# Optimization experiments

Measured on AMD Instinct MI355X. Metric: run time of the kernel, lower is better.

The kernel has to match this reference:

```python
import jax, jax.numpy as jnp
import numpy as np

C = 256
DF = 8
CQK = C // DF  # 32


def setup_inputs() -> dict:
    key = jax.random.key(0)
    ks = jax.random.split(key, 7)
    s = 0.02
    x = jax.random.normal(ks[0], (4, C, 64, 64), dtype=jnp.float32)
    Wq = jax.random.normal(ks[1], (CQK, C), dtype=jnp.float32) * s
    bq = jnp.zeros((CQK,), dtype=jnp.float32)
    Wk = jax.random.normal(ks[2], (CQK, C), dtype=jnp.float32) * s
    bk = jnp.zeros((CQK,), dtype=jnp.float32)
    Wv = jax.random.normal(ks[3], (C, C), dtype=jnp.float32) * s
    bv = jnp.zeros((C,), dtype=jnp.float32)
    gamma = jnp.ones((1,), dtype=jnp.float32)  # nonzero so output is nontrivial
    return {"x": x, "Wq": Wq, "bq": bq, "Wk": Wk, "bk": bk, "Wv": Wv, "bv": bv, "gamma": gamma}


def reference(x, Wq, bq, Wk, bk, Wv, bv, gamma):
    B, Cc, H, W = x.shape
    # flatten spatial: [B, N, C] with N = H*W
    xf = x.reshape(B, Cc, H * W).transpose(0, 2, 1)
    # 1x1 convs == per-pixel linear projections
    q = jnp.einsum('bnc,dc->bnd', xf, Wq) + bq        # [B, N, Cqk]
    k = jnp.einsum('bnc,dc->bnd', xf, Wk) + bk        # [B, N, Cqk]
    v = jnp.einsum('bnc,dc->bnd', xf, Wv) + bv        # [B, N, C]
    energy = jnp.einsum('bnd,bmd->bnm', q, k)          # [B, N, N], no scale (as in source)
    attn = jax.nn.softmax(energy, axis=-1)
    out = jnp.einsum('bnm,bmc->bnc', attn, v)          # [B, N, C]
    out = out.transpose(0, 2, 1).reshape(B, Cc, H, W)
    return gamma[0] * out
```

## Files before the change

### kernel.cpp

```cpp
#include <hip/hip_runtime.h>
#include <hip/hip_bf16.h>


typedef __attribute__((ext_vector_type(8))) short s8v;
typedef __attribute__((ext_vector_type(4))) float f4v;

#define NPIX 4096
#define CIN 256
#define DQK 32

#if __has_builtin(__builtin_amdgcn_exp2f)
#define EXP2(x) __builtin_amdgcn_exp2f(x)
#else
#define EXP2(x) exp2f(x)
#endif

#if __has_builtin(__builtin_amdgcn_s_waitcnt)
#define LGKM0_BARRIER() { __builtin_amdgcn_s_waitcnt(0xC07F); __builtin_amdgcn_s_barrier(); }
#else
#define LGKM0_BARRIER() { __asm__ __volatile__("s_waitcnt lgkmcnt(0)\n\ts_barrier" ::: "memory"); }
#endif

static __device__ __forceinline__ unsigned short f2bf(float f) {
    union { float f; unsigned int u; } v; v.f = f;
    unsigned int r = v.u + 0x7FFF + ((v.u >> 16) & 1);
    return (unsigned short)(r >> 16);
}
static __device__ __forceinline__ unsigned int fbits(float f) {
    union { float f; unsigned int u; } v; v.f = f; return v.u;
}

__global__ void wcast_kernel(const float* __restrict__ Wq, const float* __restrict__ bq,
                             const float* __restrict__ Wk, const float* __restrict__ bk,
                             const float* __restrict__ Wv, const float* __restrict__ bv,
                             unsigned short* __restrict__ Wall, float* __restrict__ ball) {
    int row = blockIdx.x;
    int t = threadIdx.x;
    const float* src; const float* bsrc;
    if (row < 32)       { src = Wq + row * 256;        bsrc = bq + row; }
    else if (row < 64)  { src = Wk + (row - 32) * 256; bsrc = bk + (row - 32); }
    else                { src = Wv + (row - 64) * 256; bsrc = bv + (row - 64); }
    Wall[row * 256 + t] = f2bf(src[t]);
    if (t == 0) ball[row] = bsrc[0];
}

__global__ void tcast_kernel(const float* __restrict__ x, unsigned short* __restrict__ xT) {
    __shared__ unsigned short tile[64][65];
    int bidx = blockIdx.x;
    int b    = bidx >> 8;
    int cblk = (bidx >> 6) & 3;
    int nblk = bidx & 63;
    int t = threadIdx.x;
    int c0 = cblk * 64, n0 = nblk * 64;
    const float* xb = x + (size_t)b * CIN * NPIX;
    #pragma unroll
    for (int p = 0; p < 4; p++) {
        int cl = p * 16 + (t >> 4);
        int nl = (t & 15) * 4;
        float4 v = *(const float4*)(xb + (size_t)(c0 + cl) * NPIX + n0 + nl);
        tile[cl][nl + 0] = f2bf(v.x);
        tile[cl][nl + 1] = f2bf(v.y);
        tile[cl][nl + 2] = f2bf(v.z);
        tile[cl][nl + 3] = f2bf(v.w);
    }
    __syncthreads();
    unsigned short* xTb = xT + (size_t)b * NPIX * CIN;
    #pragma unroll
    for (int p = 0; p < 4; p++) {
        int nl = p * 16 + (t >> 4);
        int cl = (t & 15) * 4;
        ushort4 wv;
        wv.x = tile[cl + 0][nl];
        wv.y = tile[cl + 1][nl];
        wv.z = tile[cl + 2][nl];
        wv.w = tile[cl + 3][nl];
        *(ushort4*)(xTb + (size_t)(n0 + nl) * CIN + c0 + cl) = wv;
    }
}

__global__ __launch_bounds__(256)
void proj_kernel(const unsigned short* __restrict__ xT,
                 const unsigned short* __restrict__ Wall,
                 const float* __restrict__ ball,
                 unsigned short* __restrict__ Q,
                 unsigned short* __restrict__ Kp,
                 unsigned short* __restrict__ Vt) {
    int idx  = blockIdx.x;
    int b    = (idx & 7) >> 1;
    int nblk = ((idx >> 3) << 1) | (idx & 1);
    int w    = threadIdx.x >> 6;
    int lane = threadIdx.x & 63;
    int l16 = lane & 15, quad = lane >> 4;
    int n0 = nblk * 64 + w * 16;

    const unsigned short* brow = xT + (size_t)(b * NPIX + n0 + l16) * CIN + quad * 8;
    s8v bfr[8];
    #pragma unroll
    for (int kk = 0; kk < 8; kk++) bfr[kk] = *(const s8v*)(brow + kk * 32);

    #pragma unroll
    for (int p = 0; p < 10; p++) {
        const unsigned short* w0 = Wall + (size_t)(2 * p * 16 + l16) * CIN + quad * 8;
        const unsigned short* w1 = w0 + 16 * CIN;
        f4v a0 = {0.f, 0.f, 0.f, 0.f}, a1 = {0.f, 0.f, 0.f, 0.f};
        if (p < 2) {
            #pragma unroll
            for (int kk = 0; kk < 8; kk++) {
                a0 = __builtin_amdgcn_mfma_f32_16x16x32_bf16(bfr[kk], *(const s8v*)(w0 + kk * 32), a0, 0, 0, 0);
                a1 = __builtin_amdgcn_mfma_f32_16x16x32_bf16(bfr[kk], *(const s8v*)(w1 + kk * 32), a1, 0, 0, 0);
            }
        } else {
            #pragma unroll
            for (int kk = 0; kk < 8; kk++) {
                a0 = __builtin_amdgcn_mfma_f32_16x16x32_bf16(*(const s8v*)(w0 + kk * 32), bfr[kk], a0, 0, 0, 0);
                a1 = __builtin_amdgcn_mfma_f32_16x16x32_bf16(*(const s8v*)(w1 + kk * 32), bfr[kk], a1, 0, 0, 0);
            }
        }
        #pragma unroll
        for (int half = 0; half < 2; half++) {
            int ob = 2 * p + half;
            f4v acc = half ? a1 : a0;
            if (ob < 2) {
                int oc = ob * 16 + l16;
                float bias = ball[oc];
                #pragma unroll
                for (int r = 0; r < 4; r++) {
                    int n = n0 + quad * 4 + r;
                    Q[(size_t)(b * NPIX + n) * DQK + oc] =
                        f2bf((acc[r] + bias) * 1.44269504f);
                }
            } else if (ob < 4) {
                int oc = (ob - 2) * 16 + l16;
                float bias = ball[32 + oc];
                #pragma unroll
                for (int r = 0; r < 4; r++) {
                    int n = n0 + quad * 4 + r;
                    int pn = (n & ~31) | (((n >> 2) & 1) << 4) | (((n >> 3) & 3) << 2) | (n & 3);
                    Kp[(size_t)(b * NPIX + pn) * DQK + oc] = f2bf(acc[r] + bias);
                }
            } else {
                int n = n0 + l16;
                #pragma unroll
                for (int r = 0; r < 4; r++) {
                    int ch = (ob - 4) * 16 + quad * 4 + r;
                    Vt[((size_t)b * CIN + ch) * NPIX + n] = f2bf(acc[r] + ball[64 + ch]);
                }
            }
        }
    }
}

#define ATTN_STEP(S, WB, KC0, KC1, VC, KN0, KN1, VN)                            \
    {                                                                           \
        const int kvn = ((S) + 1) & 63;                                         \
        KN0 = *(const s8v*)(kbase + (size_t)(kvn * 64) * DQK);                  \
        KN1 = *(const s8v*)(kbase + (size_t)(kvn * 64 + 16) * DQK);             \
        _Pragma("unroll")                                                       \
        for (int ct = 0; ct < 4; ct++)                                          \
            VN[ct] = *(const s8v*)(vbase + (size_t)ct * 16 * NPIX + (S) * 64);  \
        const unsigned int* rb = smemw + khw + (1 - (WB)) * 1024;               \
        s8v pa0 = (cj == 0) ? ppv : *(const s8v*)(rb + rdo0);                   \
        s8v pa1 = (cj == 1) ? ppv : *(const s8v*)(rb + rdo1);                   \
        s8v pa2 = (cj == 2) ? ppv : *(const s8v*)(rb + rdo2);                   \
        s8v pa3 = (cj == 3) ? ppv : *(const s8v*)(rb + rdo3);                   \
        f4v s0 = {0.f, 0.f, 0.f, 0.f}, s1 = {0.f, 0.f, 0.f, 0.f};               \
        s0 = __builtin_amdgcn_mfma_f32_16x16x32_bf16(KC0, qf, s0, 0, 0, 0);     \
        s1 = __builtin_amdgcn_mfma_f32_16x16x32_bf16(KC1, qf, s1, 0, 0, 0);     \
        float p00 = EXP2(s0[0]), p01 = EXP2(s0[1]);                             \
        float p02 = EXP2(s0[2]), p03 = EXP2(s0[3]);                             \
        float p10 = EXP2(s1[0]), p11 = EXP2(s1[1]);                             \
        float p12 = EXP2(s1[2]), p13 = EXP2(s1[3]);                             \
        lsum += ((p00 + p01) + (p02 + p03)) + ((p10 + p11) + (p12 + p13));      \
        union { uint4 u; s8v v; } pp;                                           \
        pp.u.x = __builtin_amdgcn_perm(fbits(p01), fbits(p00), 0x07060302);     \
        pp.u.y = __builtin_amdgcn_perm(fbits(p03), fbits(p02), 0x07060302);     \
        pp.u.z = __builtin_amdgcn_perm(fbits(p11), fbits(p10), 0x07060302);     \
        pp.u.w = __builtin_amdgcn_perm(fbits(p13), fbits(p12), 0x07060302);     \
        *(uint4*)(smemw + khw + (WB) * 1024 + wro) = pp.u;                      \
        _Pragma("unroll")                                                       \
        for (int ct = 0; ct < 4; ct++) {                                        \
            O[0][ct] = __builtin_amdgcn_mfma_f32_16x16x32_bf16(VC[ct], pa0, O[0][ct], 0, 0, 0); \
            O[1][ct] = __builtin_amdgcn_mfma_f32_16x16x32_bf16(VC[ct], pa1, O[1][ct], 0, 0, 0); \
            O[2][ct] = __builtin_amdgcn_mfma_f32_16x16x32_bf16(VC[ct], pa2, O[2][ct], 0, 0, 0); \
            O[3][ct] = __builtin_amdgcn_mfma_f32_16x16x32_bf16(VC[ct], pa3, O[3][ct], 0, 0, 0); \
        }                                                                       \
        LGKM0_BARRIER();                                                        \
        ppv = pp.v;                                                             \
    }

__global__ __launch_bounds__(512)
void attn_kernel(const unsigned short* __restrict__ Q,
                 const unsigned short* __restrict__ Kp,
                 const unsigned short* __restrict__ Vt,
                 const float* __restrict__ gamma,
                 float* __restrict__ out) {
    __shared__ __align__(16) char smem[70144];
    unsigned int* smemw = (unsigned int*)smem;

    int idx = blockIdx.x;
    int b      = (idx & 7) >> 1;
    int rowblk = ((idx >> 3) << 1) | (idx & 1);

    int lane = threadIdx.x & 63;
    int w    = threadIdx.x >> 6;
    int l16 = lane & 15, quad = lane >> 4;
    int kh = w >> 2;
    int cj = w & 3;

    const unsigned short* Kb = Kp + (size_t)b * NPIX * DQK;
    const unsigned short* Vb = Vt + (size_t)b * CIN * NPIX;

    int rowbase = rowblk * 64;
    const s8v qf = *(const s8v*)(Q + (size_t)(b * NPIX + rowbase + cj * 16 + l16) * DQK + quad * 8);

    const unsigned short* kbase = Kb + (32 * kh + l16) * DQK + quad * 8;
    const unsigned short* vbase = Vb + (size_t)(cj * 64 + l16) * NPIX + 32 * kh + quad * 8;

    const int khw  = kh * 2048;
    const int wro  = l16 * 64 + (((cj * 4 + quad) ^ (l16 & 7)) << 2);
    const int rdo0 = l16 * 64 + (((0 * 4 + quad) ^ (l16 & 7)) << 2);
    const int rdo1 = l16 * 64 + (((1 * 4 + quad) ^ (l16 & 7)) << 2);
    const int rdo2 = l16 * 64 + (((2 * 4 + quad) ^ (l16 & 7)) << 2);
    const int rdo3 = l16 * 64 + (((3 * 4 + quad) ^ (l16 & 7)) << 2);

    f4v O[4][4];
    #pragma unroll
    for (int rt = 0; rt < 4; rt++)
        #pragma unroll
        for (int ct = 0; ct < 4; ct++) O[rt][ct] = (f4v){0.f, 0.f, 0.f, 0.f};
    float lsum = 0.f;
    s8v ppv;

    s8v Kc0, Kc1, Kn0, Kn1, Vc[4], Vn[4];
    Kc0 = *(const s8v*)(kbase);
    Kc1 = *(const s8v*)(kbase + 16 * DQK);

    {
        Kn0 = *(const s8v*)(kbase + (size_t)64 * DQK);
        Kn1 = *(const s8v*)(kbase + (size_t)80 * DQK);
        #pragma unroll
        for (int ct = 0; ct < 4; ct++)
            Vc[ct] = *(const s8v*)(vbase + (size_t)ct * 16 * NPIX);
        f4v s0 = {0.f, 0.f, 0.f, 0.f}, s1 = {0.f, 0.f, 0.f, 0.f};
        s0 = __builtin_amdgcn_mfma_f32_16x16x32_bf16(Kc0, qf, s0, 0, 0, 0);
        s1 = __builtin_amdgcn_mfma_f32_16x16x32_bf16(Kc1, qf, s1, 0, 0, 0);
        float p00 = EXP2(s0[0]), p01 = EXP2(s0[1]);
        float p02 = EXP2(s0[2]), p03 = EXP2(s0[3]);
        float p10 = EXP2(s1[0]), p11 = EXP2(s1[1]);
        float p12 = EXP2(s1[2]), p13 = EXP2(s1[3]);
        lsum += ((p00 + p01) + (p02 + p03)) + ((p10 + p11) + (p12 + p13));
        union { uint4 u; s8v v; } pp;
        pp.u.x = __builtin_amdgcn_perm(fbits(p01), fbits(p00), 0x07060302);
        pp.u.y = __builtin_amdgcn_perm(fbits(p03), fbits(p02), 0x07060302);
        pp.u.z = __builtin_amdgcn_perm(fbits(p11), fbits(p10), 0x07060302);
        pp.u.w = __builtin_amdgcn_perm(fbits(p13), fbits(p12), 0x07060302);
        *(uint4*)(smemw + khw + 0 * 1024 + wro) = pp.u;
        LGKM0_BARRIER();
        ppv = pp.v;
    }

    for (int p = 0; p < 31; p++) {
        int s1i = 2 * p + 1;
        ATTN_STEP(s1i,     1, Kn0, Kn1, Vc, Kc0, Kc1, Vn);
        ATTN_STEP(s1i + 1, 0, Kc0, Kc1, Vn, Kn0, Kn1, Vc);
    }
    ATTN_STEP(63, 1, Kn0, Kn1, Vc, Kc0, Kc1, Vn);

    {
        const unsigned int* rb = smemw + khw + 1024;
        s8v pa0 = (cj == 0) ? ppv : *(const s8v*)(rb + rdo0);
        s8v pa1 = (cj == 1) ? ppv : *(const s8v*)(rb + rdo1);
        s8v pa2 = (cj == 2) ? ppv : *(const s8v*)(rb + rdo2);
        s8v pa3 = (cj == 3) ? ppv : *(const s8v*)(rb + rdo3);
        #pragma unroll
        for (int ct = 0; ct < 4; ct++) {
            O[0][ct] = __builtin_amdgcn_mfma_f32_16x16x32_bf16(Vn[ct], pa0, O[0][ct], 0, 0, 0);
            O[1][ct] = __builtin_amdgcn_mfma_f32_16x16x32_bf16(Vn[ct], pa1, O[1][ct], 0, 0, 0);
            O[2][ct] = __builtin_amdgcn_mfma_f32_16x16x32_bf16(Vn[ct], pa2, O[2][ct], 0, 0, 0);
            O[3][ct] = __builtin_amdgcn_mfma_f32_16x16x32_bf16(Vn[ct], pa3, O[3][ct], 0, 0, 0);
        }
    }

    lsum += __shfl_xor(lsum, 16);
    lsum += __shfl_xor(lsum, 32);

    __syncthreads();

    float (*ldsO)[64][68] = (float (*)[64][68])smem;
    float* ldsL = (float*)(smem + 69632);

    if (quad == 0) ldsL[kh * 64 + cj * 16 + l16] = lsum;
    if (kh == 1) {
        #pragma unroll
        for (int rt = 0; rt < 4; rt++)
            #pragma unroll
            for (int ct = 0; ct < 4; ct++)
                *(f4v*)&ldsO[cj][lane][(rt * 4 + ct) * 4] = O[rt][ct];
    }
    __syncthreads();

    if (kh == 0) {
        float g = gamma[0];
        float rinv[4];
        #pragma unroll
        for (int rt = 0; rt < 4; rt++)
            rinv[rt] = g / (ldsL[rt * 16 + l16] + ldsL[64 + rt * 16 + l16]);
        #pragma unroll
        for (int rt = 0; rt < 4; rt++) {
            #pragma unroll
            for (int ct = 0; ct < 4; ct++) {
                f4v o2 = *(const f4v*)&ldsO[cj][lane][(rt * 4 + ct) * 4];
                #pragma unroll
                for (int r = 0; r < 4; r++) {
                    int ch = cj * 64 + ct * 16 + quad * 4 + r;
                    out[((size_t)b * CIN + ch) * NPIX + rowbase + rt * 16 + l16] =
                        (O[rt][ct][r] + o2[r]) * rinv[rt];
                }
            }
        }
    }
}

extern "C" void kernel_launch(void* const* d_in, const int* in_sizes, int n_in,
                              void* d_out, int out_size, void* d_ws, size_t ws_size,
                              hipStream_t stream) {
    const float* x     = (const float*)d_in[0];
    const float* Wq    = (const float*)d_in[1];
    const float* bq    = (const float*)d_in[2];
    const float* Wk    = (const float*)d_in[3];
    const float* bk    = (const float*)d_in[4];
    const float* Wv    = (const float*)d_in[5];
    const float* bv    = (const float*)d_in[6];
    const float* gamma = (const float*)d_in[7];
    float* out = (float*)d_out;

    char* p = (char*)d_ws;
    unsigned short* xT   = (unsigned short*)p; p += (size_t)4 * NPIX * CIN * 2;
    unsigned short* Qb   = (unsigned short*)p; p += (size_t)4 * NPIX * DQK * 2;
    unsigned short* Kb   = (unsigned short*)p; p += (size_t)4 * NPIX * DQK * 2;
    unsigned short* Vt   = (unsigned short*)p; p += (size_t)4 * CIN * NPIX * 2;
    unsigned short* Wall = (unsigned short*)p; p += (size_t)320 * 256 * 2;
    float*          ball = (float*)p;          p += (size_t)320 * 4;

    wcast_kernel<<<320, 256, 0, stream>>>(Wq, bq, Wk, bk, Wv, bv, Wall, ball);
    tcast_kernel<<<1024, 256, 0, stream>>>(x, xT);
    proj_kernel<<<256, 256, 0, stream>>>(xT, Wall, ball, Qb, Kb, Vt);
    attn_kernel<<<256, 512, 0, stream>>>(Qb, Kb, Vt, gamma, out);
}
```

Baseline: 183.4 us.

## Repartition attention waves by query row tile to eliminate LDS P exchange

Each wave now owns one 16-row query tile and all 256 output channels instead of one 64-channel slice of all 64 rows. It uses its own softmax probabilities directly as the MFMA operand, which removes the LDS write/read of P and the per-step barrier. In exchange each wave loads the full V window (16 fragments per step) straight from global memory without prefetching, raising per-wave V traffic fourfold. The epilogue merges the two key halves in two rounds to fit the smaller LDS buffer.

```diff
diff --git a/kernel.cpp b/kernel.cpp
--- a/kernel.cpp
+++ b/kernel.cpp
@@ -13,12 +13,6 @@
 #define EXP2(x) __builtin_amdgcn_exp2f(x)
 #else
 #define EXP2(x) exp2f(x)
-#endif
-
-#if __has_builtin(__builtin_amdgcn_s_waitcnt)
-#define LGKM0_BARRIER() { __builtin_amdgcn_s_waitcnt(0xC07F); __builtin_amdgcn_s_barrier(); }
-#else
-#define LGKM0_BARRIER() { __asm__ __volatile__("s_waitcnt lgkmcnt(0)\n\ts_barrier" ::: "memory"); }
 #endif
 
 static __device__ __forceinline__ unsigned short f2bf(float f) {
@@ -150,19 +144,11 @@
     }
 }
 
-#define ATTN_STEP(S, WB, KC0, KC1, VC, KN0, KN1, VN)                            \
+#define ATTN_STEP(S, KC0, KC1, KN0, KN1)                                        \
     {                                                                           \
         const int kvn = ((S) + 1) & 63;                                         \
         KN0 = *(const s8v*)(kbase + (size_t)(kvn * 64) * DQK);                  \
         KN1 = *(const s8v*)(kbase + (size_t)(kvn * 64 + 16) * DQK);             \
-        _Pragma("unroll")                                                       \
-        for (int ct = 0; ct < 4; ct++)                                          \
-            VN[ct] = *(const s8v*)(vbase + (size_t)ct * 16 * NPIX + (S) * 64);  \
-        const unsigned int* rb = smemw + khw + (1 - (WB)) * 1024;               \
-        s8v pa0 = (cj == 0) ? ppv : *(const s8v*)(rb + rdo0);                   \
-        s8v pa1 = (cj == 1) ? ppv : *(const s8v*)(rb + rdo1);                   \
-        s8v pa2 = (cj == 2) ? ppv : *(const s8v*)(rb + rdo2);                   \
-        s8v pa3 = (cj == 3) ? ppv : *(const s8v*)(rb + rdo3);                   \
         f4v s0 = {0.f, 0.f, 0.f, 0.f}, s1 = {0.f, 0.f, 0.f, 0.f};               \
         s0 = __builtin_amdgcn_mfma_f32_16x16x32_bf16(KC0, qf, s0, 0, 0, 0);     \
         s1 = __builtin_amdgcn_mfma_f32_16x16x32_bf16(KC1, qf, s1, 0, 0, 0);     \
@@ -176,16 +162,12 @@
         pp.u.y = __builtin_amdgcn_perm(fbits(p03), fbits(p02), 0x07060302);     \
         pp.u.z = __builtin_amdgcn_perm(fbits(p11), fbits(p10), 0x07060302);     \
         pp.u.w = __builtin_amdgcn_perm(fbits(p13), fbits(p12), 0x07060302);     \
-        *(uint4*)(smemw + khw + (WB) * 1024 + wro) = pp.u;                      \
+        const unsigned short* vwin = vbase + (S) * 64;                          \
         _Pragma("unroll")                                                       \
-        for (int ct = 0; ct < 4; ct++) {                                        \
-            O[0][ct] = __builtin_amdgcn_mfma_f32_16x16x32_bf16(VC[ct], pa0, O[0][ct], 0, 0, 0); \
-            O[1][ct] = __builtin_amdgcn_mfma_f32_16x16x32_bf16(VC[ct], pa1, O[1][ct], 0, 0, 0); \
-            O[2][ct] = __builtin_amdgcn_mfma_f32_16x16x32_bf16(VC[ct], pa2, O[2][ct], 0, 0, 0); \
-            O[3][ct] = __builtin_amdgcn_mfma_f32_16x16x32_bf16(VC[ct], pa3, O[3][ct], 0, 0, 0); \
+        for (int ct = 0; ct < 16; ct++) {                                       \
+            s8v vf = *(const s8v*)(vwin + (size_t)ct * 16 * NPIX);              \
+            O[ct] = __builtin_amdgcn_mfma_f32_16x16x32_bf16(vf, pp.v, O[ct], 0, 0, 0); \
         }                                                                       \
-        LGKM0_BARRIER();                                                        \
-        ppv = pp.v;                                                             \
     }
 
 __global__ __launch_bounds__(512)
@@ -194,8 +176,7 @@
                  const unsigned short* __restrict__ Vt,
                  const float* __restrict__ gamma,
                  float* __restrict__ out) {
-    __shared__ __align__(16) char smem[70144];
-    unsigned int* smemw = (unsigned int*)smem;
+    __shared__ __align__(16) char smem[35328];
 
     int idx = blockIdx.x;
     int b      = (idx & 7) >> 1;
@@ -205,119 +186,62 @@
     int w    = threadIdx.x >> 6;
     int l16 = lane & 15, quad = lane >> 4;
     int kh = w >> 2;
-    int cj = w & 3;
+    int rt = w & 3;
 
     const unsigned short* Kb = Kp + (size_t)b * NPIX * DQK;
     const unsigned short* Vb = Vt + (size_t)b * CIN * NPIX;
 
     int rowbase = rowblk * 64;
-    const s8v qf = *(const s8v*)(Q + (size_t)(b * NPIX + rowbase + cj * 16 + l16) * DQK + quad * 8);
+    const s8v qf = *(const s8v*)(Q + (size_t)(b * NPIX + rowbase + rt * 16 + l16) * DQK + quad * 8);
 
     const unsigned short* kbase = Kb + (32 * kh + l16) * DQK + quad * 8;
-    const unsigned short* vbase = Vb + (size_t)(cj * 64 + l16) * NPIX + 32 * kh + quad * 8;
-
-    const int khw  = kh * 2048;
-    const int wro  = l16 * 64 + (((cj * 4 + quad) ^ (l16 & 7)) << 2);
-    const int rdo0 = l16 * 64 + (((0 * 4 + quad) ^ (l16 & 7)) << 2);
-    const int rdo1 = l16 * 64 + (((1 * 4 + quad) ^ (l16 & 7)) << 2);
-    const int rdo2 = l16 * 64 + (((2 * 4 + quad) ^ (l16 & 7)) << 2);
-    const int rdo3 = l16 * 64 + (((3 * 4 + quad) ^ (l16 & 7)) << 2);
-
-    f4v O[4][4];
-    #pragma unroll
-    for (int rt = 0; rt < 4; rt++)
-        #pragma unroll
-        for (int ct = 0; ct < 4; ct++) O[rt][ct] = (f4v){0.f, 0.f, 0.f, 0.f};
+    const unsigned short* vbase = Vb + (size_t)l16 * NPIX + 32 * kh + quad * 8;
+
+    f4v O[16];
+    #pragma unroll
+    for (int ct = 0; ct < 16; ct++) O[ct] = (f4v){0.f, 0.f, 0.f, 0.f};
     float lsum = 0.f;
-    s8v ppv;
-
-    s8v Kc0, Kc1, Kn0, Kn1, Vc[4], Vn[4];
+
+    s8v Kc0, Kc1, Kn0, Kn1;
     Kc0 = *(const s8v*)(kbase);
     Kc1 = *(const s8v*)(kbase + 16 * DQK);
 
-    {
-        Kn0 = *(const s8v*)(kbase + (size_t)64 * DQK);
-        Kn1 = *(const s8v*)(kbase + (size_t)80 * DQK);
-        #pragma unroll
-        for (int ct = 0; ct < 4; ct++)
-            Vc[ct] = *(const s8v*)(vbase + (size_t)ct * 16 * NPIX);
-        f4v s0 = {0.f, 0.f, 0.f, 0.f}, s1 = {0.f, 0.f, 0.f, 0.f};
-        s0 = __builtin_amdgcn_mfma_f32_16x16x32_bf16(Kc0, qf, s0, 0, 0, 0);
-        s1 = __builtin_amdgcn_mfma_f32_16x16x32_bf16(Kc1, qf, s1, 0, 0, 0);
-        float p00 = EXP2(s0[0]), p01 = EXP2(s0[1]);
-        float p02 = EXP2(s0[2]), p03 = EXP2(s0[3]);
-        float p10 = EXP2(s1[0]), p11 = EXP2(s1[1]);
-        float p12 = EXP2(s1[2]), p13 = EXP2(s1[3]);
-        lsum += ((p00 + p01) + (p02 + p03)) + ((p10 + p11) + (p12 + p13));
-        union { uint4 u; s8v v; } pp;
-        pp.u.x = __builtin_amdgcn_perm(fbits(p01), fbits(p00), 0x07060302);
-        pp.u.y = __builtin_amdgcn_perm(fbits(p03), fbits(p02), 0x07060302);
-        pp.u.z = __builtin_amdgcn_perm(fbits(p11), fbits(p10), 0x07060302);
-        pp.u.w = __builtin_amdgcn_perm(fbits(p13), fbits(p12), 0x07060302);
-        *(uint4*)(smemw + khw + 0 * 1024 + wro) = pp.u;
-        LGKM0_BARRIER();
-        ppv = pp.v;
-    }
-
-    for (int p = 0; p < 31; p++) {
-        int s1i = 2 * p + 1;
-        ATTN_STEP(s1i,     1, Kn0, Kn1, Vc, Kc0, Kc1, Vn);
-        ATTN_STEP(s1i + 1, 0, Kc0, Kc1, Vn, Kn0, Kn1, Vc);
-    }
-    ATTN_STEP(63, 1, Kn0, Kn1, Vc, Kc0, Kc1, Vn);
-
-    {
-        const unsigned int* rb = smemw + khw + 1024;
-        s8v pa0 = (cj == 0) ? ppv : *(const s8v*)(rb + rdo0);
-        s8v pa1 = (cj == 1) ? ppv : *(const s8v*)(rb + rdo1);
-        s8v pa2 = (cj == 2) ? ppv : *(const s8v*)(rb + rdo2);
-        s8v pa3 = (cj == 3) ? ppv : *(const s8v*)(rb + rdo3);
-        #pragma unroll
-        for (int ct = 0; ct < 4; ct++) {
-            O[0][ct] = __builtin_amdgcn_mfma_f32_16x16x32_bf16(Vn[ct], pa0, O[0][ct], 0, 0, 0);
-            O[1][ct] = __builtin_amdgcn_mfma_f32_16x16x32_bf16(Vn[ct], pa1, O[1][ct], 0, 0, 0);
-            O[2][ct] = __builtin_amdgcn_mfma_f32_16x16x32_bf16(Vn[ct], pa2, O[2][ct], 0, 0, 0);
-            O[3][ct] = __builtin_amdgcn_mfma_f32_16x16x32_bf16(Vn[ct], pa3, O[3][ct], 0, 0, 0);
-        }
+    for (int p = 0; p < 32; p++) {
+        ATTN_STEP(2 * p,     Kc0, Kc1, Kn0, Kn1);
+        ATTN_STEP(2 * p + 1, Kn0, Kn1, Kc0, Kc1);
     }
 
     lsum += __shfl_xor(lsum, 16);
     lsum += __shfl_xor(lsum, 32);
 
-    __syncthreads();
-
     float (*ldsO)[64][68] = (float (*)[64][68])smem;
-    float* ldsL = (float*)(smem + 69632);
-
-    if (quad == 0) ldsL[kh * 64 + cj * 16 + l16] = lsum;
-    if (kh == 1) {
-        #pragma unroll
-        for (int rt = 0; rt < 4; rt++)
-            #pragma unroll
-            for (int ct = 0; ct < 4; ct++)
-                *(f4v*)&ldsO[cj][lane][(rt * 4 + ct) * 4] = O[rt][ct];
-    }
-    __syncthreads();
-
-    if (kh == 0) {
-        float g = gamma[0];
-        float rinv[4];
-        #pragma unroll
-        for (int rt = 0; rt < 4; rt++)
-            rinv[rt] = g / (ldsL[rt * 16 + l16] + ldsL[64 + rt * 16 + l16]);
-        #pragma unroll
-        for (int rt = 0; rt < 4; rt++) {
-            #pragma unroll
-            for (int ct = 0; ct < 4; ct++) {
-                f4v o2 = *(const f4v*)&ldsO[cj][lane][(rt * 4 + ct) * 4];
-                #pragma unroll
-                for (int r = 0; r < 4; r++) {
-                    int ch = cj * 64 + ct * 16 + quad * 4 + r;
+    float* ldsL = (float*)(smem + 34816);
+
+    if (quad == 0) ldsL[(kh * 4 + rt) * 16 + l16] = lsum;
+
+    #pragma unroll
+    for (int rnd = 0; rnd < 2; rnd++) {
+        if (kh == 1 && (rt >> 1) == rnd) {
+            #pragma unroll
+            for (int ct = 0; ct < 16; ct++)
+                *(f4v*)&ldsO[rt & 1][lane][ct * 4] = O[ct];
+        }
+        __syncthreads();
+        if (kh == 0 && (rt >> 1) == rnd) {
+            float g = gamma[0];
+            float rinv = g / (ldsL[rt * 16 + l16] + ldsL[(4 + rt) * 16 + l16]);
+            #pragma unroll
+            for (int ct = 0; ct < 16; ct++) {
+                f4v o2 = *(const f4v*)&ldsO[rt & 1][lane][ct * 4];
+                #pragma unroll
+                for (int r = 0; r < 4; r++) {
+                    int ch = ct * 16 + quad * 4 + r;
                     out[((size_t)b * CIN + ch) * NPIX + rowbase + rt * 16 + l16] =
-                        (O[rt][ct][r] + o2[r]) * rinv[rt];
-                }
-            }
-        }
+                        (O[ct][r] + o2[r]) * rinv;
+                }
+            }
+        }
+        __syncthreads();
     }
 }
 
```

Result: slower. 419.9 us (+128.9%).

## Merge weight and input cast kernels; split projection across four block groups

Applied to the files above, without the earlier changes.

Folds the weight-cast and input transpose-cast kernels into one launch, selected by block index, which removes one kernel launch and its gap. The projection kernel is launched with four times as many blocks, and each group computes a subset of the output channel tiles (Q/K, or a slice of V). This is meant to fill more compute units than the original 256 blocks did. In exchange, every block reloads the same xT fragments, so input reads from global memory go up fourfold.

```diff
diff --git a/kernel.cpp b/kernel.cpp
--- a/kernel.cpp
+++ b/kernel.cpp
@@ -30,27 +30,28 @@
     union { float f; unsigned int u; } v; v.f = f; return v.u;
 }
 
-__global__ void wcast_kernel(const float* __restrict__ Wq, const float* __restrict__ bq,
-                             const float* __restrict__ Wk, const float* __restrict__ bk,
-                             const float* __restrict__ Wv, const float* __restrict__ bv,
-                             unsigned short* __restrict__ Wall, float* __restrict__ ball) {
-    int row = blockIdx.x;
+__global__ void prep_kernel(const float* __restrict__ Wq, const float* __restrict__ bq,
+                            const float* __restrict__ Wk, const float* __restrict__ bk,
+                            const float* __restrict__ Wv, const float* __restrict__ bv,
+                            unsigned short* __restrict__ Wall, float* __restrict__ ball,
+                            const float* __restrict__ x, unsigned short* __restrict__ xT) {
+    __shared__ unsigned short tile[64][65];
+    int blk = blockIdx.x;
     int t = threadIdx.x;
-    const float* src; const float* bsrc;
-    if (row < 32)       { src = Wq + row * 256;        bsrc = bq + row; }
-    else if (row < 64)  { src = Wk + (row - 32) * 256; bsrc = bk + (row - 32); }
-    else                { src = Wv + (row - 64) * 256; bsrc = bv + (row - 64); }
-    Wall[row * 256 + t] = f2bf(src[t]);
-    if (t == 0) ball[row] = bsrc[0];
-}
-
-__global__ void tcast_kernel(const float* __restrict__ x, unsigned short* __restrict__ xT) {
-    __shared__ unsigned short tile[64][65];
-    int bidx = blockIdx.x;
+    if (blk < 320) {
+        int row = blk;
+        const float* src; const float* bsrc;
+        if (row < 32)       { src = Wq + row * 256;        bsrc = bq + row; }
+        else if (row < 64)  { src = Wk + (row - 32) * 256; bsrc = bk + (row - 32); }
+        else                { src = Wv + (row - 64) * 256; bsrc = bv + (row - 64); }
+        Wall[row * 256 + t] = f2bf(src[t]);
+        if (t == 0) ball[row] = bsrc[0];
+        return;
+    }
+    int bidx = blk - 320;
     int b    = bidx >> 8;
     int cblk = (bidx >> 6) & 3;
     int nblk = bidx & 63;
-    int t = threadIdx.x;
     int c0 = cblk * 64, n0 = nblk * 64;
     const float* xb = x + (size_t)b * CIN * NPIX;
     #pragma unroll
@@ -78,28 +79,14 @@
     }
 }
 
-__global__ __launch_bounds__(256)
-void proj_kernel(const unsigned short* __restrict__ xT,
-                 const unsigned short* __restrict__ Wall,
-                 const float* __restrict__ ball,
-                 unsigned short* __restrict__ Q,
-                 unsigned short* __restrict__ Kp,
-                 unsigned short* __restrict__ Vt) {
-    int idx  = blockIdx.x;
-    int b    = (idx & 7) >> 1;
-    int nblk = ((idx >> 3) << 1) | (idx & 1);
-    int w    = threadIdx.x >> 6;
-    int lane = threadIdx.x & 63;
-    int l16 = lane & 15, quad = lane >> 4;
-    int n0 = nblk * 64 + w * 16;
-
-    const unsigned short* brow = xT + (size_t)(b * NPIX + n0 + l16) * CIN + quad * 8;
-    s8v bfr[8];
-    #pragma unroll
-    for (int kk = 0; kk < 8; kk++) bfr[kk] = *(const s8v*)(brow + kk * 32);
-
-    #pragma unroll
-    for (int p = 0; p < 10; p++) {
+template<int PS, int PE>
+static __device__ __forceinline__ void proj_range(
+        const s8v* bfr, const unsigned short* __restrict__ Wall,
+        const float* __restrict__ ball,
+        unsigned short* __restrict__ Q, unsigned short* __restrict__ Kp,
+        unsigned short* __restrict__ Vt, int b, int n0, int l16, int quad) {
+    #pragma unroll
+    for (int p = PS; p < PE; p++) {
         const unsigned short* w0 = Wall + (size_t)(2 * p * 16 + l16) * CIN + quad * 8;
         const unsigned short* w1 = w0 + 16 * CIN;
         f4v a0 = {0.f, 0.f, 0.f, 0.f}, a1 = {0.f, 0.f, 0.f, 0.f};
@@ -148,6 +135,33 @@
             }
         }
     }
+}
+
+__global__ __launch_bounds__(256)
+void proj_kernel(const unsigned short* __restrict__ xT,
+                 const unsigned short* __restrict__ Wall,
+                 const float* __restrict__ ball,
+                 unsigned short* __restrict__ Q,
+                 unsigned short* __restrict__ Kp,
+                 unsigned short* __restrict__ Vt) {
+    int idx  = blockIdx.x & 255;
+    int pg   = blockIdx.x >> 8;
+    int b    = (idx & 7) >> 1;
+    int nblk = ((idx >> 3) << 1) | (idx & 1);
+    int w    = threadIdx.x >> 6;
+    int lane = threadIdx.x & 63;
+    int l16 = lane & 15, quad = lane >> 4;
+    int n0 = nblk * 64 + w * 16;
+
+    const unsigned short* brow = xT + (size_t)(b * NPIX + n0 + l16) * CIN + quad * 8;
+    s8v bfr[8];
+    #pragma unroll
+    for (int kk = 0; kk < 8; kk++) bfr[kk] = *(const s8v*)(brow + kk * 32);
+
+    if (pg == 0)      proj_range<0, 2>(bfr, Wall, ball, Q, Kp, Vt, b, n0, l16, quad);
+    else if (pg == 1) proj_range<2, 5>(bfr, Wall, ball, Q, Kp, Vt, b, n0, l16, quad);
+    else if (pg == 2) proj_range<5, 8>(bfr, Wall, ball, Q, Kp, Vt, b, n0, l16, quad);
+    else              proj_range<8, 10>(bfr, Wall, ball, Q, Kp, Vt, b, n0, l16, quad);
 }
 
 #define ATTN_STEP(S, WB, KC0, KC1, VC, KN0, KN1, VN)                            \
@@ -342,8 +356,7 @@
     unsigned short* Wall = (unsigned short*)p; p += (size_t)320 * 256 * 2;
     float*          ball = (float*)p;          p += (size_t)320 * 4;
 
-    wcast_kernel<<<320, 256, 0, stream>>>(Wq, bq, Wk, bk, Wv, bv, Wall, ball);
-    tcast_kernel<<<1024, 256, 0, stream>>>(x, xT);
-    proj_kernel<<<256, 256, 0, stream>>>(xT, Wall, ball, Qb, Kb, Vt);
+    prep_kernel<<<1344, 256, 0, stream>>>(Wq, bq, Wk, bk, Wv, bv, Wall, ball, x, xT);
+    proj_kernel<<<1024, 256, 0, stream>>>(xT, Wall, ball, Qb, Kb, Vt);
     attn_kernel<<<256, 512, 0, stream>>>(Qb, Kb, Vt, gamma, out);
 }
```

New measurement: 185.2 us. Within noise of the previous version (+1.0%).
